# Optimization experiments

Measured on AMD Instinct MI355X. Metric: run time of the kernel, lower is better.

## Reference

```python
import jax, jax.numpy as jnp
import numpy as np

HID = 192
EPS = 1e-5

def _bn(x, g, b):
    # BatchNorm1d, training mode: batch stats over all leading axes, biased var
    ax = tuple(range(x.ndim - 1))
    m = x.mean(axis=ax)
    v = x.var(axis=ax)
    return (x - m) * jax.lax.rsqrt(v + EPS) * g + b

def _glorot(k, shape):
    lim = np.sqrt(6.0 / (shape[0] + shape[1]))
    return jax.random.uniform(k, shape, jnp.float32, -lim, lim)

def setup_inputs() -> dict:
    key = jax.random.key(0)
    ks = jax.random.split(key, 8)
    B, N, F, C = 16, 1024, 128, 10
    x = jax.random.normal(ks[0], (B, N, F), jnp.float32)
    adj = (jax.random.uniform(ks[1], (B, N, N)) < 0.01).astype(jnp.float32)
    adj = jnp.maximum(adj, jnp.swapaxes(adj, 1, 2))
    return dict(
        x=x, adj=adj,
        bn_feat_g=jnp.ones((F,), jnp.float32), bn_feat_b=jnp.full((F,), 1e-4, jnp.float32),
        W_feat=_glorot(ks[2], (F, HID)),
        bns_conv_g=jnp.ones((3, HID), jnp.float32), bns_conv_b=jnp.full((3, HID), 1e-4, jnp.float32),
        convs_W=jnp.stack([_glorot(jax.random.fold_in(ks[3], i), (HID, HID)) for i in range(3)]),
        convs_b=jnp.zeros((3, HID), jnp.float32),
        bn_fc_g=jnp.ones((HID,), jnp.float32), bn_fc_b=jnp.full((HID,), 1e-4, jnp.float32),
        lin_W=_glorot(ks[4], (HID, HID)), lin_b=jnp.zeros((HID,), jnp.float32),
        bn_hid_g=jnp.ones((HID,), jnp.float32), bn_hid_b=jnp.full((HID,), 1e-4, jnp.float32),
        cls_W=_glorot(ks[5], (HID, 10)), cls_b=jnp.zeros((10,), jnp.float32),
    )

def reference(x, adj, bn_feat_g, bn_feat_b, W_feat, bns_conv_g, bns_conv_b,
              convs_W, convs_b, bn_fc_g, bn_fc_b, lin_W, lin_b,
              bn_hid_g, bn_hid_b, cls_W, cls_b):
    B, N, _ = x.shape
    # dense_to_sparse discards edge values -> binary edges; add remaining self loops (weight 1)
    A = (adj != 0).astype(x.dtype)
    A = jnp.maximum(A, jnp.eye(N, dtype=x.dtype))
    deg = A.sum(-1)                                   # [B,N]
    dis = jnp.where(deg > 0, deg ** -0.5, 0.0)
    A_hat = dis[:, :, None] * A * dis[:, None, :]      # D^-1/2 (A+I) D^-1/2
    h = _bn(x, bn_feat_g, bn_feat_b)
    # conv_feat has gfn=True: pure linear transform, no bias, no propagation
    h = jax.nn.relu(jnp.einsum('bnf,fh->bnh', h, W_feat))
    for i in range(convs_W.shape[0]):
        h = _bn(h, bns_conv_g[i], bns_conv_b[i])
        h = jax.nn.relu(jnp.einsum('bij,bjh->bih', A_hat, h @ convs_W[i]) + convs_b[i])
    g = h.mean(axis=1)                                 # global_mean_pool -> [B,HID]
    g = _bn(g, bn_fc_g, bn_fc_b)
    g = jax.nn.relu(g @ lin_W + lin_b)
    g = _bn(g, bn_hid_g, bn_hid_b)
    logits = g @ cls_W + cls_b
    return jax.nn.log_softmax(logits, axis=-1)
```

## Files before the change

kernel.cpp:

```cpp
#include <hip/hip_runtime.h>
#include <hip/hip_bf16.h>

#define BB 16
#define NN 1024
#define FF 128
#define HH 192
#define NROWS (BB*NN)
#define MAXC 128
#define EPSV 1e-5f

constexpr size_t OFF_H0  = 0;
constexpr size_t OFF_ZB  = OFF_H0 + (size_t)NROWS*HH/2;
constexpr size_t OFF_DIS = OFF_ZB + (size_t)NROWS*HH/2;
constexpr size_t OFF_G   = OFF_DIS + NROWS;
constexpr size_t OFF_SH  = OFF_G + BB*HH;
constexpr size_t SH_SIZE = 3*8*512;
constexpr size_t ZERO_SZ = BB*HH + SH_SIZE;
constexpr size_t OFF_XB  = OFF_SH + SH_SIZE;
constexpr size_t OFF_WPF = OFF_XB + 256*256;
constexpr size_t OFF_WPC = OFF_WPF + (size_t)HH*FF/2;
constexpr size_t OFF_BF  = OFF_WPC + (size_t)HH*HH/2;
constexpr size_t OFF_BC  = OFF_BF + HH;
constexpr size_t OFF_CNT = OFF_BC + HH;
constexpr size_t OFF_COLS= OFF_CNT + NROWS;

typedef __attribute__((ext_vector_type(8))) short short8;
typedef __attribute__((ext_vector_type(4))) float f32x4;
typedef __attribute__((ext_vector_type(4))) unsigned int u32x4;
typedef __attribute__((ext_vector_type(2))) unsigned int u32x2;

static __device__ __forceinline__ float bf(const __hip_bfloat16 v) {
    return __bfloat162float(v);
}
static __device__ __forceinline__ float ldin(const void* p, size_t i, int isf) {
    return isf ? ((const float*)p)[i]
               : __bfloat162float(((const __hip_bfloat16*)p)[i]);
}
static __host__ __device__ __forceinline__ float* stage_h(float* ws, int s ) {
    return ws + OFF_SH + (size_t)s*8*512;
}
static __device__ __forceinline__ float blo(unsigned int u) {
    union { unsigned int x; float f; } v; v.x = u << 16; return v.f;
}
static __device__ __forceinline__ float bhi(unsigned int u) {
    union { unsigned int x; float f; } v; v.x = u & 0xFFFF0000u; return v.f;
}
static __device__ __forceinline__ unsigned int packbf(float a, float b) {
    union { unsigned int u; __hip_bfloat16 h[2]; } p;
    p.h[0] = __float2bfloat16(a); p.h[1] = __float2bfloat16(b);
    return p.u;
}

template<int NTHR>
static __device__ __forceinline__ int detect_isf(const unsigned int* __restrict__ adjw,
                                                 int tid, int* sh_flag) {
    if (tid == 0) *sh_flag = 0;
    __syncthreads();
    int hit = 0;
    #pragma unroll
    for (int k = tid; k < 1024; k += NTHR)
        if ((adjw[k] & 0xFFFFu) == 0x3F80u) hit = 1;
    if (hit) *sh_flag = 1;
    __syncthreads();
    return (*sh_flag == 0) ? 1 : 0;
}

__global__ __launch_bounds__(256) void phase1(const void* __restrict__ adj,
                                              const void* __restrict__ x, float* ws) {
    __shared__ int sflag;
    int tid = threadIdx.x;
    const int isf = detect_isf<256>((const unsigned int*)adj, tid, &sflag);
    if (blockIdx.x < NROWS) {
        int row = blockIdx.x;
        if (row < 60) {
            size_t idx = (size_t)row*256 + tid;
            if (idx < ZERO_SZ) ws[OFF_G + idx] = 0.f;
        }
        int i   = row & (NN - 1);
        __shared__ int cnt_s;
        __shared__ unsigned short colbuf[MAXC];
        if (tid == 0) cnt_s = 0;
        __syncthreads();
        int j0 = tid*4;
        unsigned int bits[4];
        if (isf) {
            u32x4 v = *(const u32x4*)((const unsigned int*)adj + (size_t)row*NN + j0);
            bits[0]=v[0]; bits[1]=v[1]; bits[2]=v[2]; bits[3]=v[3];
        } else {
            u32x2 v = *(const u32x2*)((const unsigned short*)adj + (size_t)row*NN + j0);
            bits[0]=(v[0]&0xFFFFu); bits[1]=(v[0]>>16); bits[2]=(v[1]&0xFFFFu); bits[3]=(v[1]>>16);
        }
        #pragma unroll
        for (int e = 0; e < 4; ++e) {
            int j = j0 + e;
            if ((bits[e] << 1) != 0u || j == i) {
                int p = atomicAdd(&cnt_s, 1);
                if (p < MAXC) colbuf[p] = (unsigned short)j;
            }
        }
        __syncthreads();
        int c = cnt_s; if (c > MAXC) c = MAXC;
        if (tid == 0) {
            ((int*)(ws + OFF_CNT))[row] = c;
            ws[OFF_DIS + row] = rsqrtf((float)cnt_s);
        }
        unsigned short* cols = (unsigned short*)(ws + OFF_COLS);
        for (int k = tid; k < c; k += 256) cols[(size_t)row*MAXC + k] = colbuf[k];
    } else {
        int b2 = blockIdx.x - NROWS;
        int f = tid & (FF-1), half = tid >> 7;
        int r0 = b2*64 + half*32;
        float s = 0.f, sq = 0.f;
        for (int r = 0; r < 32; ++r) {
            float v = ldin(x, (size_t)(r0 + r)*FF + f, isf);
            s += v; sq += v*v;
        }
        __shared__ float xs[256];
        if (half == 1) { xs[f] = s; xs[128 + f] = sq; }
        __syncthreads();
        if (half == 0) {
            ws[OFF_XB + (size_t)b2*256 + f]       = s  + xs[f];
            ws[OFF_XB + (size_t)b2*256 + 128 + f] = sq + xs[128 + f];
        }
    }
}

__global__ __launch_bounds__(128) void prep_feat(const void* __restrict__ adj,
                          const void* __restrict__ W_feat,
                          const void* __restrict__ gg, const void* __restrict__ bb,
                          float* ws) {
    __shared__ int sflag;
    int n = blockIdx.x, k = threadIdx.x;
    const int isf = detect_isf<128>((const unsigned int*)adj, k, &sflag);
    float s = 0.f, q = 0.f;
    for (int b = 0; b < 256; ++b) {
        s += ws[OFF_XB + (size_t)b*256 + k];
        q += ws[OFF_XB + (size_t)b*256 + 128 + k];
    }
    float m   = s * (1.f/NROWS);
    float var = q * (1.f/NROWS) - m*m;
    float a   = ldin(gg, k, isf) * rsqrtf(var + EPSV);
    float c   = ldin(bb, k, isf) - m*a;
    float wv  = ldin(W_feat, (size_t)k*HH + n, isf);
    ((__hip_bfloat16*)(ws + OFF_WPF))[(size_t)n*FF + k] = __float2bfloat16(a*wv);
    __shared__ float red[FF];
    red[k] = c*wv;
    __syncthreads();
    for (int s2 = FF/2; s2 > 0; s2 >>= 1) {
        if (k < s2) red[k] += red[k + s2];
        __syncthreads();
    }
    if (k == 0) ws[OFF_BF + n] = red[0];
}

__global__ __launch_bounds__(192) void prep_conv(const void* __restrict__ adj,
                          const void* __restrict__ convs_W,
                          const void* __restrict__ gg, const void* __restrict__ bb,
                          int layer, float* ws) {
    __shared__ int sflag;
    int n = blockIdx.x, k = threadIdx.x;
    const int isf = detect_isf<192>((const unsigned int*)adj, k, &sflag);
    const float* st = stage_h(ws, layer);
    float s = 0.f, sq = 0.f;
    #pragma unroll
    for (int bkt = 0; bkt < 8; ++bkt) {
        s  += st[bkt*512 + k];
        sq += st[bkt*512 + 256 + k];
    }
    float m   = s * (1.f/NROWS);
    float var = sq * (1.f/NROWS) - m*m;
    float a   = ldin(gg, (size_t)layer*HH + k, isf) * rsqrtf(var + EPSV);
    float c   = ldin(bb, (size_t)layer*HH + k, isf) - m*a;
    float wv  = ldin(convs_W, (size_t)layer*HH*HH + (size_t)k*HH + n, isf);
    ((__hip_bfloat16*)(ws + OFF_WPC))[(size_t)n*HH + k] = __float2bfloat16(a*wv);
    __shared__ float red[HH];
    red[k] = c*wv;
    __syncthreads();
    if (k < 96) red[k] += red[k + 96];
    __syncthreads();
    for (int s2 = 48; s2 >= 3; s2 >>= 1) {
        if (k < s2) red[k] += red[k + s2];
        __syncthreads();
    }
    if (k == 0) ws[OFF_BC + n] = red[0] + red[1] + red[2];
}

template<int K, int MODE>
__global__ __launch_bounds__(256) void gemm_mfma(const void* __restrict__ adj,
                                                 const void* __restrict__ A,
                                                 const __hip_bfloat16* __restrict__ BT,
                                                 const float* __restrict__ bias,
                                                 float* __restrict__ ws) {
    __shared__ int sflag;
    int tid = threadIdx.x;
    const int isf = detect_isf<256>((const unsigned int*)adj, tid, &sflag);
    int lane = tid & 63, w = tid >> 6;
    int wr = w & 1, wc = w >> 1;
    int bi = blockIdx.x;
    int batch = bi & 15, seg = bi >> 4;
    int row0 = batch*NN + seg*32 + wr*16;
    int col0 = wc*96;
    int m    = lane & 15, quad = lane >> 4;
    f32x4 acc[6];
    #pragma unroll
    for (int t = 0; t < 6; ++t) acc[t] = f32x4{0.f,0.f,0.f,0.f};
    float bv[6];
    #pragma unroll
    for (int t = 0; t < 6; ++t) bv[t] = bias[col0 + t*16 + m];
    #pragma unroll
    for (int kb = 0; kb < K/32; ++kb) {
        short8 a;
        if (MODE == 0 && isf) {
            const float* Ar = (const float*)A + (size_t)(row0+m)*K + kb*32 + quad*8;
            f32x4 v0 = *(const f32x4*)Ar;
            f32x4 v1 = *(const f32x4*)(Ar + 4);
            union { short8 s8; __hip_bfloat16 h[8]; } u;
            #pragma unroll
            for (int e = 0; e < 4; ++e) {
                u.h[e]   = __float2bfloat16(v0[e]);
                u.h[e+4] = __float2bfloat16(v1[e]);
            }
            a = u.s8;
        } else {
            a = *(const short8*)((const __hip_bfloat16*)A +
                                 (size_t)(row0+m)*K + kb*32 + quad*8);
        }
        #pragma unroll
        for (int t = 0; t < 6; ++t) {
            short8 b = *(const short8*)(BT + (size_t)(col0 + t*16+m)*K + kb*32 + quad*8);
            acc[t] = __builtin_amdgcn_mfma_f32_16x16x32_bf16(a, b, acc[t], 0, 0, 0);
        }
    }
    if (MODE == 0) {
        __shared__ float sh[2*HH];
        for (int i = tid; i < 2*HH; i += 256) sh[i] = 0.f;
        __syncthreads();
        __hip_bfloat16* H0 = (__hip_bfloat16*)(ws + OFF_H0);
        #pragma unroll
        for (int t = 0; t < 6; ++t) {
            int ch = col0 + t*16 + m;
            float s = 0.f, sq = 0.f;
            #pragma unroll
            for (int r = 0; r < 4; ++r) {
                float o = fmaxf(acc[t][r] + bv[t], 0.f);
                H0[(size_t)(row0 + quad*4 + r)*HH + ch] = __float2bfloat16(o);
                s += o; sq += o*o;
            }
            atomicAdd(&sh[ch], s);
            atomicAdd(&sh[HH + ch], sq);
        }
        __syncthreads();
        float* st = stage_h(ws, 0) + (size_t)(bi & 7)*512;
        if (tid < HH) {
            atomicAdd(&st[tid], sh[tid]);
            atomicAdd(&st[256 + tid], sh[HH + tid]);
        }
    } else {
        const float* dis = ws + OFF_DIS;
        __hip_bfloat16* Z = (__hip_bfloat16*)(ws + OFF_ZB);
        float sc[4];
        #pragma unroll
        for (int r = 0; r < 4; ++r) sc[r] = dis[row0 + quad*4 + r];
        #pragma unroll
        for (int t = 0; t < 6; ++t)
            #pragma unroll
            for (int r = 0; r < 4; ++r)
                Z[(size_t)(row0 + quad*4 + r)*HH + col0 + t*16 + m] =
                    __float2bfloat16((acc[t][r] + bv[t]) * sc[r]);
    }
}

__global__ __launch_bounds__(512) void spmm(const void* __restrict__ adj,
                                            const void* __restrict__ bias, int layer,
                                            float* __restrict__ stat_out, int is_pool,
                                            float* ws) {
    __shared__ unsigned int Zs[NN*16];
    __shared__ int sflag;
    int tid = threadIdx.x;
    const int isf = detect_isf<512>((const unsigned int*)adj, tid, &sflag);
    int bi = blockIdx.x;
    int batch = bi & 15;
    int rest  = bi >> 4;
    int slice = rest % 6;
    int qtr   = rest / 6;
    int c0 = slice*32;
    const unsigned int* Zu = (const unsigned int*)(ws + OFF_ZB)
                             + (size_t)batch*NN*96 + c0/2;
    for (int i = tid; i < NN*16; i += 512) {
        int r = i >> 4, u = i & 15;
        Zs[i] = Zu[(size_t)r*96 + u];
    }
    __syncthreads();
    int d = tid & 7, rslot = tid >> 3;
    const float* dis = ws + OFF_DIS;
    const int* cnt = (const int*)(ws + OFF_CNT);
    const unsigned short* cols = (const unsigned short*)(ws + OFF_COLS);
    unsigned int* H0u = (unsigned int*)(ws + OFF_H0);
    float bch[4];
    #pragma unroll
    for (int e = 0; e < 4; ++e)
        bch[e] = ldin(bias, (size_t)layer*HH + c0 + d*4 + e, isf);
    float s_acc[4] = {0.f,0.f,0.f,0.f}, q_acc[4] = {0.f,0.f,0.f,0.f};
    for (int it = 0; it < 4; ++it) {
        int row = batch*NN + qtr*256 + it*64 + rslot;
        int c = cnt[row];
        const unsigned short* cl = cols + (size_t)row*MAXC;
        float a0=0.f, a1=0.f, a2=0.f, a3=0.f;
        int k = 0;
        for (; k + 8 <= c; k += 8) {
            u32x4 cw = *(const u32x4*)(cl + k);
            int j[8];
            j[0]=(int)(cw[0]&0xFFFFu); j[1]=(int)(cw[0]>>16);
            j[2]=(int)(cw[1]&0xFFFFu); j[3]=(int)(cw[1]>>16);
            j[4]=(int)(cw[2]&0xFFFFu); j[5]=(int)(cw[2]>>16);
            j[6]=(int)(cw[3]&0xFFFFu); j[7]=(int)(cw[3]>>16);
            u32x2 z[8];
            #pragma unroll
            for (int e = 0; e < 8; ++e)
                z[e] = *(const u32x2*)(&Zs[j[e]*16 + d*2]);
            #pragma unroll
            for (int e = 0; e < 8; ++e) {
                a0 += blo(z[e][0]); a1 += bhi(z[e][0]);
                a2 += blo(z[e][1]); a3 += bhi(z[e][1]);
            }
        }
        for (; k < c; ++k) {
            u32x2 z = *(const u32x2*)(&Zs[(int)cl[k]*16 + d*2]);
            a0 += blo(z[0]); a1 += bhi(z[0]);
            a2 += blo(z[1]); a3 += bhi(z[1]);
        }
        float dd = dis[row];
        float o0 = fmaxf(dd*a0 + bch[0], 0.f);
        float o1 = fmaxf(dd*a1 + bch[1], 0.f);
        float o2 = fmaxf(dd*a2 + bch[2], 0.f);
        float o3 = fmaxf(dd*a3 + bch[3], 0.f);
        u32x2 outw; outw[0] = packbf(o0,o1); outw[1] = packbf(o2,o3);
        *(u32x2*)(&H0u[(size_t)row*96 + c0/2 + d*2]) = outw;
        s_acc[0]+=o0; s_acc[1]+=o1; s_acc[2]+=o2; s_acc[3]+=o3;
        q_acc[0]+=o0*o0; q_acc[1]+=o1*o1; q_acc[2]+=o2*o2; q_acc[3]+=o3*o3;
    }
    #pragma unroll
    for (int e = 0; e < 4; ++e) {
        #pragma unroll
        for (int mask = 8; mask < 64; mask <<= 1) {
            s_acc[e] += __shfl_xor(s_acc[e], mask, 64);
            q_acc[e] += __shfl_xor(q_acc[e], mask, 64);
        }
    }
    if ((tid & 63) < 8) {
        if (is_pool) {
            #pragma unroll
            for (int e = 0; e < 4; ++e)
                atomicAdd(&ws[OFF_G + (size_t)batch*HH + c0 + d*4 + e], s_acc[e]);
        } else {
            float* st = stat_out + (bi & 7)*512;
            #pragma unroll
            for (int e = 0; e < 4; ++e) {
                atomicAdd(&st[c0 + d*4 + e],       s_acc[e]);
                atomicAdd(&st[256 + c0 + d*4 + e], q_acc[e]);
            }
        }
    }
}

__global__ __launch_bounds__(768) void tail(const void* __restrict__ adj,
                     const void* __restrict__ fc_g,  const void* __restrict__ fc_b,
                     const void* __restrict__ lin_W, const void* __restrict__ lin_b,
                     const void* __restrict__ hid_g, const void* __restrict__ hid_b,
                     const void* __restrict__ cls_W, const void* __restrict__ cls_b,
                     void* __restrict__ out, const float* ws) {
    __shared__ float g1[BB][HH];
    __shared__ float g2[BB][HH];
    __shared__ __hip_bfloat16 Wl[HH*HH];
    __shared__ float logits[BB][10];
    __shared__ float lse[BB];
    __shared__ int sflag;
    int tid = threadIdx.x;
    const int isf = detect_isf<768>((const unsigned int*)adj, tid, &sflag);
    const float* g = ws + OFF_G;
    if (isf) {
        const f32x4* Wp = (const f32x4*)lin_W;
        for (int i = tid; i < HH*HH/8; i += 768) {
            f32x4 v0 = Wp[2*i], v1 = Wp[2*i + 1];
            union { short8 s8; __hip_bfloat16 h[8]; } u;
            #pragma unroll
            for (int e = 0; e < 4; ++e) {
                u.h[e]   = __float2bfloat16(v0[e]);
                u.h[e+4] = __float2bfloat16(v1[e]);
            }
            *(short8*)&Wl[8*i] = u.s8;
        }
    } else {
        const short8* Wp = (const short8*)lin_W;
        for (int i = tid; i < HH*HH/8; i += 768)
            *(short8*)&Wl[8*i] = Wp[i];
    }
    if (tid < HH) {
        float s = 0.f, sq = 0.f;
        for (int b = 0; b < BB; ++b) {
            float v = g[b*HH + tid] * (1.f/NN);
            s += v; sq += v*v;
        }
        float m = s*(1.f/BB), var = sq*(1.f/BB) - m*m;
        float a = ldin(fc_g, tid, isf) * rsqrtf(var + EPSV);
        float c = ldin(fc_b, tid, isf) - m*a;
        for (int b = 0; b < BB; ++b) g1[b][tid] = g[b*HH + tid]*(1.f/NN)*a + c;
    }
    __syncthreads();
    {
        int b = tid / 48, grp = tid - b*48;
        int n0 = grp*4;
        float acc[4];
        #pragma unroll
        for (int e = 0; e < 4; ++e) acc[e] = ldin(lin_b, n0 + e, isf);
        for (int k = 0; k < HH; ++k) {
            float gv = g1[b][k];
            u32x2 wz = *(const u32x2*)&Wl[k*HH + n0];
            acc[0] += gv * blo(wz[0]); acc[1] += gv * bhi(wz[0]);
            acc[2] += gv * blo(wz[1]); acc[3] += gv * bhi(wz[1]);
        }
        #pragma unroll
        for (int e = 0; e < 4; ++e) g2[b][n0 + e] = fmaxf(acc[e], 0.f);
    }
    __syncthreads();
    if (tid < HH) {
        float s = 0.f, sq = 0.f;
        for (int b = 0; b < BB; ++b) { float v = g2[b][tid]; s += v; sq += v*v; }
        float m = s*(1.f/BB), var = sq*(1.f/BB) - m*m;
        float a = ldin(hid_g, tid, isf) * rsqrtf(var + EPSV);
        float c = ldin(hid_b, tid, isf) - m*a;
        for (int b = 0; b < BB; ++b) g2[b][tid] = g2[b][tid]*a + c;
    }
    __syncthreads();
    if (tid < BB*10) {
        int b = tid/10, k = tid%10;
        float acc = ldin(cls_b, k, isf);
        for (int h = 0; h < HH; ++h) acc += g2[b][h] * ldin(cls_W, (size_t)h*10 + k, isf);
        logits[b][k] = acc;
    }
    __syncthreads();
    if (tid < BB) {
        float m = -1e30f;
        for (int k = 0; k < 10; ++k) m = fmaxf(m, logits[tid][k]);
        float s = 0.f;
        for (int k = 0; k < 10; ++k) s += expf(logits[tid][k] - m);
        lse[tid] = m + logf(s);
    }
    __syncthreads();
    if (tid < BB*10) {
        int b = tid/10;
        float v = logits[b][tid%10] - lse[b];
        if (isf) ((float*)out)[tid] = v;
        else     ((__hip_bfloat16*)out)[tid] = __float2bfloat16(v);
    }
}

extern "C" void kernel_launch(void* const* d_in, const int* in_sizes, int n_in,
                              void* d_out, int out_size, void* d_ws, size_t ws_size,
                              hipStream_t stream) {
    const void* x       = d_in[0];
    const void* adj     = d_in[1];
    const void* bnf_g   = d_in[2];
    const void* bnf_b   = d_in[3];
    const void* W_feat  = d_in[4];
    const void* bnc_g   = d_in[5];
    const void* bnc_b   = d_in[6];
    const void* convs_W = d_in[7];
    const void* convs_b = d_in[8];
    const void* fc_g    = d_in[9];
    const void* fc_b    = d_in[10];
    const void* lin_W   = d_in[11];
    const void* lin_b   = d_in[12];
    const void* hid_g   = d_in[13];
    const void* hid_b   = d_in[14];
    const void* cls_W   = d_in[15];
    const void* cls_b   = d_in[16];

    float* ws = (float*)d_ws;
    const __hip_bfloat16* WPF = (const __hip_bfloat16*)(ws + OFF_WPF);
    const __hip_bfloat16* WPC = (const __hip_bfloat16*)(ws + OFF_WPC);

    phase1<<<NROWS + 256, 256, 0, stream>>>(adj, x, ws);
    prep_feat<<<HH, FF, 0, stream>>>(adj, W_feat, bnf_g, bnf_b, ws);
    gemm_mfma<FF, 0><<<NROWS/32, 256, 0, stream>>>(adj, x, WPF, ws + OFF_BF, ws);
    for (int l = 0; l < 3; ++l) {
        prep_conv<<<HH, HH, 0, stream>>>(adj, convs_W, bnc_g, bnc_b, l, ws);
        gemm_mfma<HH, 1><<<NROWS/32, 256, 0, stream>>>(
            adj, (const void*)(ws + OFF_H0), WPC, ws + OFF_BC, ws);
        spmm<<<384, 512, 0, stream>>>(adj, convs_b, l,
            (l < 2) ? stage_h(ws, l + 1) : nullptr, (l == 2) ? 1 : 0, ws);
    }
    tail<<<1, 768, 0, stream>>>(adj, fc_g, fc_b, lin_W, lin_b,
                                hid_g, hid_b, cls_W, cls_b, d_out, ws);
}
```

Measured before the change: 314.2 us.

## Fold BatchNorm scaling into GEMM prologue and drop separate prep kernels

```diff
diff --git a/kernel.cpp b/kernel.cpp
--- a/kernel.cpp
+++ b/kernel.cpp
@@ -17,11 +17,9 @@
 constexpr size_t SH_SIZE = 3*8*512;
 constexpr size_t ZERO_SZ = BB*HH + SH_SIZE;
 constexpr size_t OFF_XB  = OFF_SH + SH_SIZE;
-constexpr size_t OFF_WPF = OFF_XB + 256*256;
+constexpr size_t OFF_WPF = OFF_XB + 32*256;
 constexpr size_t OFF_WPC = OFF_WPF + (size_t)HH*FF/2;
-constexpr size_t OFF_BF  = OFF_WPC + (size_t)HH*HH/2;
-constexpr size_t OFF_BC  = OFF_BF + HH;
-constexpr size_t OFF_CNT = OFF_BC + HH;
+constexpr size_t OFF_CNT = OFF_WPC + (size_t)3*HH*HH/2;
 constexpr size_t OFF_COLS= OFF_CNT + NROWS;
 
 typedef __attribute__((ext_vector_type(8))) short short8;
@@ -66,52 +64,61 @@
 }
 
 __global__ __launch_bounds__(256) void phase1(const void* __restrict__ adj,
-                                              const void* __restrict__ x, float* ws) {
+                                              const void* __restrict__ x,
+                                              const void* __restrict__ W_feat,
+                                              const void* __restrict__ convs_W,
+                                              float* ws) {
     __shared__ int sflag;
     int tid = threadIdx.x;
     const int isf = detect_isf<256>((const unsigned int*)adj, tid, &sflag);
-    if (blockIdx.x < NROWS) {
-        int row = blockIdx.x;
-        if (row < 60) {
-            size_t idx = (size_t)row*256 + tid;
+    int bi = blockIdx.x;
+    if (bi < NROWS/4) {
+        if (bi < 60) {
+            size_t idx = (size_t)bi*256 + tid;
             if (idx < ZERO_SZ) ws[OFF_G + idx] = 0.f;
         }
+        __shared__ int cnt_s[4];
+        __shared__ unsigned short colbuf[4*MAXC];
+        int r4 = tid >> 6, tl = tid & 63;
+        int row = bi*4 + r4;
         int i   = row & (NN - 1);
-        __shared__ int cnt_s;
-        __shared__ unsigned short colbuf[MAXC];
-        if (tid == 0) cnt_s = 0;
+        if (tl == 0) cnt_s[r4] = 0;
         __syncthreads();
-        int j0 = tid*4;
-        unsigned int bits[4];
-        if (isf) {
-            u32x4 v = *(const u32x4*)((const unsigned int*)adj + (size_t)row*NN + j0);
-            bits[0]=v[0]; bits[1]=v[1]; bits[2]=v[2]; bits[3]=v[3];
-        } else {
-            u32x2 v = *(const u32x2*)((const unsigned short*)adj + (size_t)row*NN + j0);
-            bits[0]=(v[0]&0xFFFFu); bits[1]=(v[0]>>16); bits[2]=(v[1]&0xFFFFu); bits[3]=(v[1]>>16);
-        }
-        #pragma unroll
-        for (int e = 0; e < 4; ++e) {
-            int j = j0 + e;
-            if ((bits[e] << 1) != 0u || j == i) {
-                int p = atomicAdd(&cnt_s, 1);
-                if (p < MAXC) colbuf[p] = (unsigned short)j;
+        #pragma unroll
+        for (int p = 0; p < 4; ++p) {
+            int j0 = p*256 + tl*4;
+            unsigned int bits[4];
+            if (isf) {
+                u32x4 v = *(const u32x4*)((const unsigned int*)adj + (size_t)row*NN + j0);
+                bits[0]=v[0]; bits[1]=v[1]; bits[2]=v[2]; bits[3]=v[3];
+            } else {
+                u32x2 v = *(const u32x2*)((const unsigned short*)adj + (size_t)row*NN + j0);
+                bits[0]=(v[0]&0xFFFFu); bits[1]=(v[0]>>16);
+                bits[2]=(v[1]&0xFFFFu); bits[3]=(v[1]>>16);
+            }
+            #pragma unroll
+            for (int e = 0; e < 4; ++e) {
+                int j = j0 + e;
+                if ((bits[e] << 1) != 0u || j == i) {
+                    int p2 = atomicAdd(&cnt_s[r4], 1);
+                    if (p2 < MAXC) colbuf[r4*MAXC + p2] = (unsigned short)j;
+                }
             }
         }
         __syncthreads();
-        int c = cnt_s; if (c > MAXC) c = MAXC;
-        if (tid == 0) {
+        int c = cnt_s[r4]; if (c > MAXC) c = MAXC;
+        if (tl == 0) {
             ((int*)(ws + OFF_CNT))[row] = c;
-            ws[OFF_DIS + row] = rsqrtf((float)cnt_s);
+            ws[OFF_DIS + row] = rsqrtf((float)cnt_s[r4]);
         }
         unsigned short* cols = (unsigned short*)(ws + OFF_COLS);
-        for (int k = tid; k < c; k += 256) cols[(size_t)row*MAXC + k] = colbuf[k];
-    } else {
-        int b2 = blockIdx.x - NROWS;
+        for (int k = tl; k < c; k += 64) cols[(size_t)row*MAXC + k] = colbuf[r4*MAXC + k];
+    } else if (bi < NROWS/4 + 32) {
+        int b2 = bi - NROWS/4;
         int f = tid & (FF-1), half = tid >> 7;
-        int r0 = b2*64 + half*32;
+        int r0 = b2*512 + half*256;
         float s = 0.f, sq = 0.f;
-        for (int r = 0; r < 32; ++r) {
+        for (int r = 0; r < 256; ++r) {
             float v = ldin(x, (size_t)(r0 + r)*FF + f, isf);
             s += v; sq += v*v;
         }
@@ -122,78 +129,65 @@
             ws[OFF_XB + (size_t)b2*256 + f]       = s  + xs[f];
             ws[OFF_XB + (size_t)b2*256 + 128 + f] = sq + xs[128 + f];
         }
-    }
-}
-
-__global__ __launch_bounds__(128) void prep_feat(const void* __restrict__ adj,
-                          const void* __restrict__ W_feat,
-                          const void* __restrict__ gg, const void* __restrict__ bb,
-                          float* ws) {
-    __shared__ int sflag;
-    int n = blockIdx.x, k = threadIdx.x;
-    const int isf = detect_isf<128>((const unsigned int*)adj, k, &sflag);
-    float s = 0.f, q = 0.f;
-    for (int b = 0; b < 256; ++b) {
-        s += ws[OFF_XB + (size_t)b*256 + k];
-        q += ws[OFF_XB + (size_t)b*256 + 128 + k];
-    }
-    float m   = s * (1.f/NROWS);
-    float var = q * (1.f/NROWS) - m*m;
-    float a   = ldin(gg, k, isf) * rsqrtf(var + EPSV);
-    float c   = ldin(bb, k, isf) - m*a;
-    float wv  = ldin(W_feat, (size_t)k*HH + n, isf);
-    ((__hip_bfloat16*)(ws + OFF_WPF))[(size_t)n*FF + k] = __float2bfloat16(a*wv);
-    __shared__ float red[FF];
-    red[k] = c*wv;
-    __syncthreads();
-    for (int s2 = FF/2; s2 > 0; s2 >>= 1) {
-        if (k < s2) red[k] += red[k + s2];
-        __syncthreads();
-    }
-    if (k == 0) ws[OFF_BF + n] = red[0];
-}
-
-__global__ __launch_bounds__(192) void prep_conv(const void* __restrict__ adj,
-                          const void* __restrict__ convs_W,
-                          const void* __restrict__ gg, const void* __restrict__ bb,
-                          int layer, float* ws) {
-    __shared__ int sflag;
-    int n = blockIdx.x, k = threadIdx.x;
-    const int isf = detect_isf<192>((const unsigned int*)adj, k, &sflag);
-    const float* st = stage_h(ws, layer);
-    float s = 0.f, sq = 0.f;
-    #pragma unroll
-    for (int bkt = 0; bkt < 8; ++bkt) {
-        s  += st[bkt*512 + k];
-        sq += st[bkt*512 + 256 + k];
-    }
-    float m   = s * (1.f/NROWS);
-    float var = sq * (1.f/NROWS) - m*m;
-    float a   = ldin(gg, (size_t)layer*HH + k, isf) * rsqrtf(var + EPSV);
-    float c   = ldin(bb, (size_t)layer*HH + k, isf) - m*a;
-    float wv  = ldin(convs_W, (size_t)layer*HH*HH + (size_t)k*HH + n, isf);
-    ((__hip_bfloat16*)(ws + OFF_WPC))[(size_t)n*HH + k] = __float2bfloat16(a*wv);
-    __shared__ float red[HH];
-    red[k] = c*wv;
-    __syncthreads();
-    if (k < 96) red[k] += red[k + 96];
-    __syncthreads();
-    for (int s2 = 48; s2 >= 3; s2 >>= 1) {
-        if (k < s2) red[k] += red[k + s2];
-        __syncthreads();
-    }
-    if (k == 0) ws[OFF_BC + n] = red[0] + red[1] + red[2];
+    } else {
+        int t = bi - NROWS/4 - 32;
+        int mat = t / 48, stripe = t % 48, n0 = stripe*4;
+        if (mat == 0) {
+            __hip_bfloat16* wpf = (__hip_bfloat16*)(ws + OFF_WPF);
+            for (int idx = tid; idx < 4*FF; idx += 256) {
+                int nl = idx >> 7, k = idx & (FF-1);
+                wpf[(size_t)(n0+nl)*FF + k] =
+                    __float2bfloat16(ldin(W_feat, (size_t)k*HH + n0 + nl, isf));
+            }
+        } else {
+            int l = mat - 1;
+            __hip_bfloat16* wpc = (__hip_bfloat16*)(ws + OFF_WPC);
+            for (int idx = tid; idx < 4*HH; idx += 256) {
+                int nl = idx / HH, k = idx - nl*HH;
+                wpc[(size_t)l*HH*HH + (size_t)(n0+nl)*HH + k] =
+                    __float2bfloat16(ldin(convs_W, (size_t)l*HH*HH + (size_t)k*HH + n0 + nl, isf));
+            }
+        }
+    }
 }
 
 template<int K, int MODE>
 __global__ __launch_bounds__(256) void gemm_mfma(const void* __restrict__ adj,
                                                  const void* __restrict__ A,
                                                  const __hip_bfloat16* __restrict__ BT,
-                                                 const float* __restrict__ bias,
+                                                 const void* __restrict__ g_src,
+                                                 const void* __restrict__ b_src,
+                                                 int layer,
                                                  float* __restrict__ ws) {
     __shared__ int sflag;
+    __shared__ float afold[K], cfold[K], biasS[HH];
     int tid = threadIdx.x;
     const int isf = detect_isf<256>((const unsigned int*)adj, tid, &sflag);
+    if (tid < K) {
+        float s = 0.f, q = 0.f;
+        if (MODE == 0) {
+            for (int b = 0; b < 32; ++b) {
+                s += ws[OFF_XB + (size_t)b*256 + tid];
+                q += ws[OFF_XB + (size_t)b*256 + 128 + tid];
+            }
+        } else {
+            const float* st = stage_h(ws, layer);
+            #pragma unroll
+            for (int b = 0; b < 8; ++b) { s += st[b*512 + tid]; q += st[b*512 + 256 + tid]; }
+        }
+        float m = s * (1.f/NROWS);
+        float var = q * (1.f/NROWS) - m*m;
+        float a = ldin(g_src, (size_t)layer*K + tid, isf) * rsqrtf(var + EPSV);
+        afold[tid] = a;
+        cfold[tid] = ldin(b_src, (size_t)layer*K + tid, isf) - m*a;
+    }
+    __syncthreads();
+    if (tid < HH) {
+        float b = 0.f;
+        for (int k = 0; k < K; ++k) b += cfold[k] * bf(BT[(size_t)tid*K + k]);
+        biasS[tid] = b;
+    }
+    __syncthreads();
     int lane = tid & 63, w = tid >> 6;
     int wr = w & 1, wc = w >> 1;
     int bi = blockIdx.x;
@@ -206,24 +200,34 @@
     for (int t = 0; t < 6; ++t) acc[t] = f32x4{0.f,0.f,0.f,0.f};
     float bv[6];
     #pragma unroll
-    for (int t = 0; t < 6; ++t) bv[t] = bias[col0 + t*16 + m];
+    for (int t = 0; t < 6; ++t) bv[t] = biasS[col0 + t*16 + m];
     #pragma unroll
     for (int kb = 0; kb < K/32; ++kb) {
+        int k0 = kb*32 + quad*8;
+        f32x4 af0 = *(const f32x4*)&afold[k0];
+        f32x4 af1 = *(const f32x4*)&afold[k0 + 4];
         short8 a;
         if (MODE == 0 && isf) {
-            const float* Ar = (const float*)A + (size_t)(row0+m)*K + kb*32 + quad*8;
+            const float* Ar = (const float*)A + (size_t)(row0+m)*K + k0;
             f32x4 v0 = *(const f32x4*)Ar;
             f32x4 v1 = *(const f32x4*)(Ar + 4);
             union { short8 s8; __hip_bfloat16 h[8]; } u;
             #pragma unroll
             for (int e = 0; e < 4; ++e) {
-                u.h[e]   = __float2bfloat16(v0[e]);
-                u.h[e+4] = __float2bfloat16(v1[e]);
+                u.h[e]   = __float2bfloat16(v0[e]*af0[e]);
+                u.h[e+4] = __float2bfloat16(v1[e]*af1[e]);
             }
             a = u.s8;
         } else {
-            a = *(const short8*)((const __hip_bfloat16*)A +
-                                 (size_t)(row0+m)*K + kb*32 + quad*8);
+            union { short8 s8; __hip_bfloat16 h[8]; } u, v;
+            u.s8 = *(const short8*)((const __hip_bfloat16*)A +
+                                    (size_t)(row0+m)*K + k0);
+            #pragma unroll
+            for (int e = 0; e < 4; ++e) {
+                v.h[e]   = __float2bfloat16(bf(u.h[e])  *af0[e]);
+                v.h[e+4] = __float2bfloat16(bf(u.h[e+4])*af1[e]);
+            }
+            a = v.s8;
         }
         #pragma unroll
         for (int t = 0; t < 6; ++t) {
@@ -480,13 +484,12 @@
     const __hip_bfloat16* WPF = (const __hip_bfloat16*)(ws + OFF_WPF);
     const __hip_bfloat16* WPC = (const __hip_bfloat16*)(ws + OFF_WPC);
 
-    phase1<<<NROWS + 256, 256, 0, stream>>>(adj, x, ws);
-    prep_feat<<<HH, FF, 0, stream>>>(adj, W_feat, bnf_g, bnf_b, ws);
-    gemm_mfma<FF, 0><<<NROWS/32, 256, 0, stream>>>(adj, x, WPF, ws + OFF_BF, ws);
+    phase1<<<NROWS/4 + 32 + 192, 256, 0, stream>>>(adj, x, W_feat, convs_W, ws);
+    gemm_mfma<FF, 0><<<NROWS/32, 256, 0, stream>>>(adj, x, WPF, bnf_g, bnf_b, 0, ws);
     for (int l = 0; l < 3; ++l) {
-        prep_conv<<<HH, HH, 0, stream>>>(adj, convs_W, bnc_g, bnc_b, l, ws);
         gemm_mfma<HH, 1><<<NROWS/32, 256, 0, stream>>>(
-            adj, (const void*)(ws + OFF_H0), WPC, ws + OFF_BC, ws);
+            adj, (const void*)(ws + OFF_H0), WPC + (size_t)l*HH*HH,
+            bnc_g, bnc_b, l, ws);
         spmm<<<384, 512, 0, stream>>>(adj, convs_b, l,
             (l < 2) ? stage_h(ws, l + 1) : nullptr, (l == 2) ? 1 : 0, ws);
     }
```

Result: slower. 343.7 us (+9.4%).
